# Performance work log

Hardware: AMD Instinct MI355X
Metric: run time of the kernel (lower is better)

The kernel has to match this reference:

```python
import jax, jax.numpy as jnp
import numpy as np

N = 1048576   # points
C = 50000     # clusters
F1, F2, FO = 128, 64, 64

def _lin(k, out_d, in_d):
    w = jax.random.normal(k, (out_d, in_d), jnp.float32) * (1.0 / np.sqrt(in_d))
    return w

def setup_inputs() -> dict:
    key = jax.random.key(0)
    ks = jax.random.split(key, 13)
    points = jax.random.normal(ks[0], (N, 3), jnp.float32)
    inv_feats = jax.random.normal(ks[1], (N, 4), jnp.float32)
    cluster = jax.random.randint(ks[2], (N,), 0, C, dtype=jnp.int32)
    return {
        "points": points, "inv_feats": inv_feats, "cluster": cluster,
        "W1": _lin(ks[3], F2, 4),       "b1": jnp.zeros((F2,), jnp.float32),
        "W2": _lin(ks[4], F1, F2),      "b2": jnp.zeros((F1,), jnp.float32),
        "W3": _lin(ks[5], F2, F1),      "b3": jnp.zeros((F2,), jnp.float32),
        "W4": _lin(ks[6], FO, F2),      "b4": jnp.zeros((FO,), jnp.float32),
        "W5": _lin(ks[7], 3, FO + 3),   "b5": jnp.zeros((3,), jnp.float32),
    }

def reference(points, inv_feats, cluster, W1, b1, W2, b2, W3, b3, W4, b4, W5, b5):
    relu = jax.nn.relu
    fc1 = relu(inv_feats @ W1.T + b1)                 # [N, F2]
    fc2 = relu(fc1 @ W2.T + b2)                       # [N, F1]
    # global_max_pool over clusters; fc2 >= 0 so clamping empty segments (-inf) to 0 is safe
    mx = jax.ops.segment_max(fc2, cluster, num_segments=C)
    mx = jnp.maximum(mx, 0.0)                         # [C, F1]
    fc3 = relu(mx @ W3.T + b3)                        # [C, F2]
    fc4 = relu(fc3 @ W4.T + b4)                       # [C, FO]
    repeated = fc4[cluster]                           # gather [N, FO]
    concat = jnp.concatenate([points, repeated], axis=-1)  # [N, FO+3]
    fc5 = relu(concat @ W5.T + b5)                    # [N, 3]
    sums = jax.ops.segment_sum(fc5, cluster, num_segments=C)
    cnt = jax.ops.segment_sum(jnp.ones((fc5.shape[0], 1), fc5.dtype), cluster, num_segments=C)
    angles = jax.nn.sigmoid(sums / jnp.maximum(cnt, 1.0))  # [C, 3]
    return (fc4, angles)
```

## Files before the change

kernel.cpp:

```cpp
#include <hip/hip_runtime.h>

#define N_PTS 1048576
#define NC 50000
#define SCAN_B 196

typedef int   i32x4  __attribute__((ext_vector_type(4)));
typedef float f32x4v __attribute__((ext_vector_type(4)));

__device__ __forceinline__ unsigned short bf16rne(float f) {
    unsigned u = __float_as_uint(f);
    u = (u + 0x7fffu + ((u >> 16) & 1u)) >> 16;
    return (unsigned short)u;
}
__device__ __forceinline__ f32x4v mfma16(i32x4 a, i32x4 b, f32x4v c) {
    asm("v_mfma_f32_16x16x32_bf16 %0, %1, %2, %0" : "+v"(c) : "v"(a), "v"(b));
    return c;
}
__device__ __forceinline__ int cvtpk(float lo, float hi) {
    int r;
    asm("v_cvt_pk_bf16_f32 %0, %1, %2" : "=v"(r) : "v"(lo), "v"(hi));
    return r;
}

#define DPPSHR(D, X) __builtin_amdgcn_update_dpp(0, (X), 0x110 | (D), 0xf, 0xf, true)
#define DPPSHL1(X)   __builtin_amdgcn_update_dpp(0, (X), 0x101, 0xf, 0xf, true)

__global__ __launch_bounds__(256) void k_histprep(
    const int* __restrict__ cluster, int* __restrict__ counts,
    const float* __restrict__ W2, const float* __restrict__ W3,
    const float* __restrict__ W4,
    unsigned short* __restrict__ W2bf, unsigned short* __restrict__ W3bf,
    unsigned short* __restrict__ W4bf)
{
    int i = blockIdx.x * 256 + threadIdx.x;
    if (i < 8192)       W2bf[i]         = bf16rne(W2[i]);
    else if (i < 16384) W3bf[i - 8192]  = bf16rne(W3[i - 8192]);
    else if (i < 20480) W4bf[i - 16384] = bf16rne(W4[i - 16384]);
    atomicAdd(counts + cluster[i], 1);
}

__device__ __forceinline__ int block_excl_scan256(int v, int* lsum, int tid) {
    const int lane = tid & 63, wv = tid >> 6;
    int x = v, u;
    u = __shfl_up(x, 1, 64);  if (lane >= 1)  x += u;
    u = __shfl_up(x, 2, 64);  if (lane >= 2)  x += u;
    u = __shfl_up(x, 4, 64);  if (lane >= 4)  x += u;
    u = __shfl_up(x, 8, 64);  if (lane >= 8)  x += u;
    u = __shfl_up(x, 16, 64); if (lane >= 16) x += u;
    u = __shfl_up(x, 32, 64); if (lane >= 32) x += u;
    if (lane == 63) lsum[wv] = x;
    __syncthreads();
    int woff = 0;
    if (wv > 0) woff += lsum[0];
    if (wv > 1) woff += lsum[1];
    if (wv > 2) woff += lsum[2];
    return woff + x - v;
}

__global__ __launch_bounds__(256) void k_scanA(
    const int* __restrict__ counts, int* __restrict__ partial)
{
    __shared__ int lsum[4];
    int i = blockIdx.x * 256 + threadIdx.x;
    int v = (i < NC) ? counts[i] : 0;
    int e = block_excl_scan256(v, lsum, threadIdx.x);
    if (threadIdx.x == 255) partial[blockIdx.x] = e + v;
}

__global__ __launch_bounds__(256) void k_scanC(
    const int* __restrict__ counts, const int* __restrict__ partial,
    int* __restrict__ cursor)
{
    __shared__ int lsum[4];
    __shared__ int tot;
    const int tid = threadIdx.x;
    int pv = (tid < SCAN_B && tid < blockIdx.x) ? partial[tid] : 0;
    int pe = block_excl_scan256(pv, lsum, tid);
    if (tid == 255) tot = pe + pv;
    __syncthreads();
    const int pref = tot;
    __syncthreads();
    int i = blockIdx.x * 256 + tid;
    int v = (i < NC) ? counts[i] : 0;
    int e = block_excl_scan256(v, lsum, tid);
    if (i < NC) cursor[i] = pref + e;
}

template<bool SORTED>
__global__ __launch_bounds__(256) void k_scatter(
    const int* __restrict__ cluster, const float* __restrict__ inv,
    const float* __restrict__ points, int* __restrict__ cursor,
    int* __restrict__ perm, int* __restrict__ pclus,
    float4* __restrict__ invs, float4* __restrict__ ptsc)
{
    int i = blockIdx.x * 256 + threadIdx.x;
    int c = cluster[i];
    int pos = atomicAdd(cursor + c, 1);
    pclus[pos] = c;
    if (SORTED) {
        invs[pos] = *(const float4*)(inv + (size_t)i * 4);
        float4 pt = { points[(size_t)i * 3 + 0], points[(size_t)i * 3 + 1],
                      points[(size_t)i * 3 + 2], 0.f };
        ptsc[pos] = pt;
    } else {
        perm[pos] = i;
    }
}

template<bool SORTED>
__global__ __launch_bounds__(256, 4) void k_points_mfma(
    const float* __restrict__ inv_feats,
    const int* __restrict__ perm, const int* __restrict__ pclus,
    const float4* __restrict__ invs,
    const float* __restrict__ W1, const float* __restrict__ b1,
    const unsigned short* __restrict__ W2bf, const float* __restrict__ b2,
    float* __restrict__ mx)
{
    const int tid  = threadIdx.x;
    const int wv   = tid >> 6;
    const int l    = tid & 63;
    const int base = (blockIdx.x * 4 + wv) * 32;
    const int m16 = l & 15;
    const int g4  = (l >> 4) * 4;
    const int k8  = (l >> 4) * 8;

    float4 xA, xB;
    if (SORTED) {
        xA = invs[base + m16];
        xB = invs[base + 16 + m16];
    } else {
        const int pA = perm[base + m16];
        const int pB = perm[base + 16 + m16];
        xA = *(const float4*)(inv_feats + (size_t)pA * 4);
        xB = *(const float4*)(inv_feats + (size_t)pB * 4);
    }

#define ROW2(K, QA, QB) float QA, QB; { \
    const float4 w = *(const float4*)(W1 + (size_t)(K) * 4); \
    const float bb = b1[K]; \
    float a = bb; \
    a = fmaf(w.x, xA.x, a); a = fmaf(w.y, xA.y, a); \
    a = fmaf(w.z, xA.z, a); a = fmaf(w.w, xA.w, a); \
    QA = fmaxf(a, 0.f); \
    float b = bb; \
    b = fmaf(w.x, xB.x, b); b = fmaf(w.y, xB.y, b); \
    b = fmaf(w.z, xB.z, b); b = fmaf(w.w, xB.w, b); \
    QB = fmaxf(b, 0.f); }

    i32x4 b00, b01, b10, b11;
    {
        ROW2(k8 + 0, qa0, qb0) ROW2(k8 + 1, qa1, qb1)
        ROW2(k8 + 2, qa2, qb2) ROW2(k8 + 3, qa3, qb3)
        ROW2(k8 + 4, qa4, qb4) ROW2(k8 + 5, qa5, qb5)
        ROW2(k8 + 6, qa6, qb6) ROW2(k8 + 7, qa7, qb7)
        b00[0] = cvtpk(qa0, qa1); b00[1] = cvtpk(qa2, qa3);
        b00[2] = cvtpk(qa4, qa5); b00[3] = cvtpk(qa6, qa7);
        b10[0] = cvtpk(qb0, qb1); b10[1] = cvtpk(qb2, qb3);
        b10[2] = cvtpk(qb4, qb5); b10[3] = cvtpk(qb6, qb7);
    }
    {
        ROW2(32 + k8 + 0, qa0, qb0) ROW2(32 + k8 + 1, qa1, qb1)
        ROW2(32 + k8 + 2, qa2, qb2) ROW2(32 + k8 + 3, qa3, qb3)
        ROW2(32 + k8 + 4, qa4, qb4) ROW2(32 + k8 + 5, qa5, qb5)
        ROW2(32 + k8 + 6, qa6, qb6) ROW2(32 + k8 + 7, qa7, qb7)
        b01[0] = cvtpk(qa0, qa1); b01[1] = cvtpk(qa2, qa3);
        b01[2] = cvtpk(qa4, qa5); b01[3] = cvtpk(qa6, qa7);
        b11[0] = cvtpk(qb0, qb1); b11[1] = cvtpk(qb2, qb3);
        b11[2] = cvtpk(qb4, qb5); b11[3] = cvtpk(qb6, qb7);
    }
#undef ROW2

    const int cp0 = pclus[base + m16] + 1;
    const int cp1 = pclus[base + 16 + m16] + 1;
    const bool e0a = (DPPSHR(1, cp0) == cp0);
    const bool e0b = (DPPSHR(2, cp0) == cp0);
    const bool e0c = (DPPSHR(4, cp0) == cp0);
    const bool e0d = (DPPSHR(8, cp0) == cp0);
    const bool tl0 = (DPPSHL1(cp0) != cp0);
    const bool e1a = (DPPSHR(1, cp1) == cp1);
    const bool e1b = (DPPSHR(2, cp1) == cp1);
    const bool e1c = (DPPSHR(4, cp1) == cp1);
    const bool e1d = (DPPSHR(8, cp1) == cp1);
    const bool tl1 = (DPPSHL1(cp1) != cp1);
    int* mrow0 = (int*)mx + (size_t)(cp0 - 1) * 128;
    int* mrow1 = (int*)mx + (size_t)(cp1 - 1) * 128;

#define LDA(MB, KK) (*(const i32x4*)(W2bf + (size_t)(kcc + (MB)*16 + m16) * 64 + (KK)*32 + k8))

#define SC4(V, EA, EB, EC, ED) { float _u; \
    _u = __int_as_float(DPPSHR(1, __float_as_int(V))); if (EA) V = fmaxf(V, _u); \
    _u = __int_as_float(DPPSHR(2, __float_as_int(V))); if (EB) V = fmaxf(V, _u); \
    _u = __int_as_float(DPPSHR(4, __float_as_int(V))); if (EC) V = fmaxf(V, _u); \
    _u = __int_as_float(DPPSHR(8, __float_as_int(V))); if (ED) V = fmaxf(V, _u); }

#define EMIT(ACC, MB, EA, EB, EC, ED, TL, MROW) { \
    const float4 bb = *(const float4*)(b2 + kcc + (MB)*16 + g4); \
    float v0 = fmaxf(ACC[0] + bb.x, 0.f); \
    float v1 = fmaxf(ACC[1] + bb.y, 0.f); \
    float v2 = fmaxf(ACC[2] + bb.z, 0.f); \
    float v3 = fmaxf(ACC[3] + bb.w, 0.f); \
    SC4(v0, EA, EB, EC, ED) SC4(v1, EA, EB, EC, ED) \
    SC4(v2, EA, EB, EC, ED) SC4(v3, EA, EB, EC, ED) \
    if (TL) { \
        if (v0 > 0.f) atomicMax(MROW + kcc + (MB)*16 + g4 + 0, __float_as_int(v0)); \
        if (v1 > 0.f) atomicMax(MROW + kcc + (MB)*16 + g4 + 1, __float_as_int(v1)); \
        if (v2 > 0.f) atomicMax(MROW + kcc + (MB)*16 + g4 + 2, __float_as_int(v2)); \
        if (v3 > 0.f) atomicMax(MROW + kcc + (MB)*16 + g4 + 3, __float_as_int(v3)); } }

#define PASS(KC) { \
    const int kcc = (KC) * 64; \
    const i32x4 a00 = LDA(0,0), a01 = LDA(0,1), a10 = LDA(1,0), a11 = LDA(1,1); \
    const i32x4 a20 = LDA(2,0), a21 = LDA(2,1), a30 = LDA(3,0), a31 = LDA(3,1); \
    f32x4v c00 = {0.f,0.f,0.f,0.f}, c01 = {0.f,0.f,0.f,0.f}; \
    f32x4v c10 = {0.f,0.f,0.f,0.f}, c11 = {0.f,0.f,0.f,0.f}; \
    f32x4v c20 = {0.f,0.f,0.f,0.f}, c21 = {0.f,0.f,0.f,0.f}; \
    f32x4v c30 = {0.f,0.f,0.f,0.f}, c31 = {0.f,0.f,0.f,0.f}; \
    c00 = mfma16(a00, b00, c00); c00 = mfma16(a01, b01, c00); \
    c10 = mfma16(a10, b00, c10); c10 = mfma16(a11, b01, c10); \
    c20 = mfma16(a20, b00, c20); c20 = mfma16(a21, b01, c20); \
    c30 = mfma16(a30, b00, c30); c30 = mfma16(a31, b01, c30); \
    c01 = mfma16(a00, b10, c01); c01 = mfma16(a01, b11, c01); \
    c11 = mfma16(a10, b10, c11); c11 = mfma16(a11, b11, c11); \
    c21 = mfma16(a20, b10, c21); c21 = mfma16(a21, b11, c21); \
    c31 = mfma16(a30, b10, c31); c31 = mfma16(a31, b11, c31); \
    EMIT(c00, 0, e0a, e0b, e0c, e0d, tl0, mrow0) \
    EMIT(c10, 1, e0a, e0b, e0c, e0d, tl0, mrow0) \
    EMIT(c20, 2, e0a, e0b, e0c, e0d, tl0, mrow0) \
    EMIT(c30, 3, e0a, e0b, e0c, e0d, tl0, mrow0) \
    EMIT(c01, 0, e1a, e1b, e1c, e1d, tl1, mrow1) \
    EMIT(c11, 1, e1a, e1b, e1c, e1d, tl1, mrow1) \
    EMIT(c21, 2, e1a, e1b, e1c, e1d, tl1, mrow1) \
    EMIT(c31, 3, e1a, e1b, e1c, e1d, tl1, mrow1) }

    PASS(0)
    PASS(1)
#undef PASS
#undef EMIT
#undef SC4
#undef LDA
}

__global__ __launch_bounds__(256, 4) void k_cluster_mfma(
    const float* __restrict__ mx,
    const unsigned short* __restrict__ W3bf, const float* __restrict__ b3,
    const unsigned short* __restrict__ W4bf, const float* __restrict__ b4,
    float* __restrict__ fc4out)
{
    __shared__ __align__(16) unsigned short f3[4][32 * 64];
    const int tid = threadIdx.x;
    const int wv  = tid >> 6;
    const int l   = tid & 63;
    const int m16 = l & 15;
    const int g4  = (l >> 4) * 4;
    const int k8  = (l >> 4) * 8;
    const int cbase = (blockIdx.x * 4 + wv) * 32;
    const int cA = cbase + m16;
    const int cB = cbase + 16 + m16;
    const size_t rA = (size_t)min(cA, NC - 1) * 128;
    const size_t rB = (size_t)min(cB, NC - 1) * 128;
    unsigned short* f3w = &f3[wv][0];
    const int swA = (m16 & 7) << 3;
    const int swB = swA;

    f32x4v d00 = {0,0,0,0}, d01 = {0,0,0,0}, d02 = {0,0,0,0}, d03 = {0,0,0,0};
    f32x4v d10 = {0,0,0,0}, d11 = {0,0,0,0}, d12 = {0,0,0,0}, d13 = {0,0,0,0};

#define LD3(MB, KK) (*(const i32x4*)(W3bf + (size_t)((MB)*16 + m16) * 128 + (KK)*32 + k8))
#define FC3STEP(KK) { \
    const float4 vA0 = *(const float4*)(mx + rA + (KK)*32 + k8); \
    const float4 vA1 = *(const float4*)(mx + rA + (KK)*32 + k8 + 4); \
    const float4 vB0 = *(const float4*)(mx + rB + (KK)*32 + k8); \
    const float4 vB1 = *(const float4*)(mx + rB + (KK)*32 + k8 + 4); \
    i32x4 bA = { cvtpk(vA0.x, vA0.y), cvtpk(vA0.z, vA0.w), \
                 cvtpk(vA1.x, vA1.y), cvtpk(vA1.z, vA1.w) }; \
    i32x4 bB = { cvtpk(vB0.x, vB0.y), cvtpk(vB0.z, vB0.w), \
                 cvtpk(vB1.x, vB1.y), cvtpk(vB1.z, vB1.w) }; \
    const i32x4 a0 = LD3(0, KK), a1 = LD3(1, KK), a2 = LD3(2, KK), a3 = LD3(3, KK); \
    d00 = mfma16(a0, bA, d00); d01 = mfma16(a1, bA, d01); \
    d02 = mfma16(a2, bA, d02); d03 = mfma16(a3, bA, d03); \
    d10 = mfma16(a0, bB, d10); d11 = mfma16(a1, bB, d11); \
    d12 = mfma16(a2, bB, d12); d13 = mfma16(a3, bB, d13); }
    FC3STEP(0) FC3STEP(1) FC3STEP(2) FC3STEP(3)
#undef FC3STEP
#undef LD3

#define ST3(DD, MB, CL, SW) { \
    const float4 bb = *(const float4*)(b3 + (MB)*16 + g4); \
    float v0 = fmaxf(DD[0] + bb.x, 0.f); \
    float v1 = fmaxf(DD[1] + bb.y, 0.f); \
    float v2 = fmaxf(DD[2] + bb.z, 0.f); \
    float v3 = fmaxf(DD[3] + bb.w, 0.f); \
    int2 pk = { cvtpk(v0, v1), cvtpk(v2, v3) }; \
    *(int2*)(f3w + (CL)*64 + ((((MB)*16 + g4)) ^ (SW))) = pk; }
    ST3(d00, 0, m16, swA) ST3(d01, 1, m16, swA) ST3(d02, 2, m16, swA) ST3(d03, 3, m16, swA)
    ST3(d10, 0, 16 + m16, swB) ST3(d11, 1, 16 + m16, swB) ST3(d12, 2, 16 + m16, swB) ST3(d13, 3, 16 + m16, swB)
#undef ST3

    f32x4v e00 = {0,0,0,0}, e01 = {0,0,0,0}, e02 = {0,0,0,0}, e03 = {0,0,0,0};
    f32x4v e10 = {0,0,0,0}, e11 = {0,0,0,0}, e12 = {0,0,0,0}, e13 = {0,0,0,0};
#define LD4(MB, KK) (*(const i32x4*)(W4bf + (size_t)((MB)*16 + m16) * 64 + (KK)*32 + k8))
#define FC4STEP(KK) { \
    const i32x4 bA4 = *(const i32x4*)(f3w + m16*64 + (((KK)*32 + k8) ^ swA)); \
    const i32x4 bB4 = *(const i32x4*)(f3w + (16 + m16)*64 + (((KK)*32 + k8) ^ swB)); \
    const i32x4 a0 = LD4(0, KK), a1 = LD4(1, KK), a2 = LD4(2, KK), a3 = LD4(3, KK); \
    e00 = mfma16(a0, bA4, e00); e01 = mfma16(a1, bA4, e01); \
    e02 = mfma16(a2, bA4, e02); e03 = mfma16(a3, bA4, e03); \
    e10 = mfma16(a0, bB4, e10); e11 = mfma16(a1, bB4, e11); \
    e12 = mfma16(a2, bB4, e12); e13 = mfma16(a3, bB4, e13); }
    FC4STEP(0) FC4STEP(1)
#undef FC4STEP
#undef LD4

#define WR(EE, MB, CL) if ((CL) < NC) { \
    const float4 bb = *(const float4*)(b4 + (MB)*16 + g4); \
    float4 o; \
    o.x = fmaxf(EE[0] + bb.x, 0.f); \
    o.y = fmaxf(EE[1] + bb.y, 0.f); \
    o.z = fmaxf(EE[2] + bb.z, 0.f); \
    o.w = fmaxf(EE[3] + bb.w, 0.f); \
    *(float4*)(fc4out + (size_t)(CL)*64 + (MB)*16 + g4) = o; }
    WR(e00, 0, cA) WR(e01, 1, cA) WR(e02, 2, cA) WR(e03, 3, cA)
    WR(e10, 0, cB) WR(e11, 1, cB) WR(e12, 2, cB) WR(e13, 3, cB)
#undef WR
}

template<bool SORTED>
__global__ __launch_bounds__(256) void k_fc5_sorted(
    const float* __restrict__ points,
    const int* __restrict__ perm, const int* __restrict__ pclus,
    const float4* __restrict__ ptsc,
    const float* __restrict__ fc4, const float* __restrict__ W5,
    const float* __restrict__ b5, float* __restrict__ sums)
{
    const int t = blockIdx.x * 256 + threadIdx.x;
    const int c = pclus[t];
    float p0, p1, p2;
    if (SORTED) {
        const float4 pt = ptsc[t];
        p0 = pt.x; p1 = pt.y; p2 = pt.z;
    } else {
        const int p = perm[t];
        p0 = points[(size_t)p * 3 + 0];
        p1 = points[(size_t)p * 3 + 1];
        p2 = points[(size_t)p * 3 + 2];
    }
    const float* f4 = fc4 + (size_t)c * 64;

    float a0 = b5[0];
    a0 = fmaf(W5[0], p0, a0); a0 = fmaf(W5[1], p1, a0); a0 = fmaf(W5[2], p2, a0);
    float a1 = b5[1];
    a1 = fmaf(W5[67], p0, a1); a1 = fmaf(W5[68], p1, a1); a1 = fmaf(W5[69], p2, a1);
    float a2 = b5[2];
    a2 = fmaf(W5[134], p0, a2); a2 = fmaf(W5[135], p1, a2); a2 = fmaf(W5[136], p2, a2);

#pragma unroll
    for (int j = 0; j < 64; j += 4) {
        float4 v = *(const float4*)(f4 + j);
        a0 = fmaf(W5[3 + j + 0], v.x, a0);
        a0 = fmaf(W5[3 + j + 1], v.y, a0);
        a0 = fmaf(W5[3 + j + 2], v.z, a0);
        a0 = fmaf(W5[3 + j + 3], v.w, a0);
        a1 = fmaf(W5[70 + j + 0], v.x, a1);
        a1 = fmaf(W5[70 + j + 1], v.y, a1);
        a1 = fmaf(W5[70 + j + 2], v.z, a1);
        a1 = fmaf(W5[70 + j + 3], v.w, a1);
        a2 = fmaf(W5[137 + j + 0], v.x, a2);
        a2 = fmaf(W5[137 + j + 1], v.y, a2);
        a2 = fmaf(W5[137 + j + 2], v.z, a2);
        a2 = fmaf(W5[137 + j + 3], v.w, a2);
    }
    a0 = fmaxf(a0, 0.f);
    a1 = fmaxf(a1, 0.f);
    a2 = fmaxf(a2, 0.f);

    const int lane = threadIdx.x & 63;
    const int cu1  = __shfl_up(c, 1, 64);
    const int cu2  = __shfl_up(c, 2, 64);
    const int cu4  = __shfl_up(c, 4, 64);
    const int cu8  = __shfl_up(c, 8, 64);
    const int cu16 = __shfl_up(c, 16, 64);
    const int cu32 = __shfl_up(c, 32, 64);
    const int cdn  = __shfl_down(c, 1, 64);
    const bool eq0 = (lane >= 1)  && (cu1  == c);
    const bool eq1 = (lane >= 2)  && (cu2  == c);
    const bool eq2 = (lane >= 4)  && (cu4  == c);
    const bool eq3 = (lane >= 8)  && (cu8  == c);
    const bool eq4 = (lane >= 16) && (cu16 == c);
    const bool eq5 = (lane >= 32) && (cu32 == c);
    const bool tail = (lane == 63) || (cdn != c);

    float u0, u1, u2;
    u0 = __shfl_up(a0, 1, 64);  u1 = __shfl_up(a1, 1, 64);  u2 = __shfl_up(a2, 1, 64);
    if (eq0) { a0 += u0; a1 += u1; a2 += u2; }
    u0 = __shfl_up(a0, 2, 64);  u1 = __shfl_up(a1, 2, 64);  u2 = __shfl_up(a2, 2, 64);
    if (eq1) { a0 += u0; a1 += u1; a2 += u2; }
    u0 = __shfl_up(a0, 4, 64);  u1 = __shfl_up(a1, 4, 64);  u2 = __shfl_up(a2, 4, 64);
    if (eq2) { a0 += u0; a1 += u1; a2 += u2; }
    u0 = __shfl_up(a0, 8, 64);  u1 = __shfl_up(a1, 8, 64);  u2 = __shfl_up(a2, 8, 64);
    if (eq3) { a0 += u0; a1 += u1; a2 += u2; }
    u0 = __shfl_up(a0, 16, 64); u1 = __shfl_up(a1, 16, 64); u2 = __shfl_up(a2, 16, 64);
    if (eq4) { a0 += u0; a1 += u1; a2 += u2; }
    u0 = __shfl_up(a0, 32, 64); u1 = __shfl_up(a1, 32, 64); u2 = __shfl_up(a2, 32, 64);
    if (eq5) { a0 += u0; a1 += u1; a2 += u2; }

    if (tail) {
        float* srow = sums + (size_t)c * 3;
        atomicAdd(srow + 0, a0);
        atomicAdd(srow + 1, a1);
        atomicAdd(srow + 2, a2);
    }
}

__global__ __launch_bounds__(256) void k_angles(
    const float* __restrict__ sums, const int* __restrict__ counts,
    float* __restrict__ angout)
{
    int c = blockIdx.x * 256 + threadIdx.x;
    if (c >= NC) return;
    const float cnt = fmaxf((float)counts[c], 1.f);
#pragma unroll
    for (int r = 0; r < 3; ++r) {
        float s = sums[(size_t)c * 3 + r] / cnt;
        angout[(size_t)c * 3 + r] = 1.f / (1.f + expf(-s));
    }
}

extern "C" void kernel_launch(void* const* d_in, const int* in_sizes, int n_in,
                              void* d_out, int out_size, void* d_ws, size_t ws_size,
                              hipStream_t stream) {
    const float* points  = (const float*)d_in[0];
    const float* inv     = (const float*)d_in[1];
    const int*   cluster = (const int*)d_in[2];
    const float* W1 = (const float*)d_in[3];
    const float* b1 = (const float*)d_in[4];
    const float* W2 = (const float*)d_in[5];
    const float* b2 = (const float*)d_in[6];
    const float* W3 = (const float*)d_in[7];
    const float* b3 = (const float*)d_in[8];
    const float* W4 = (const float*)d_in[9];
    const float* b4 = (const float*)d_in[10];
    const float* W5 = (const float*)d_in[11];
    const float* b5 = (const float*)d_in[12];

    float* out    = (float*)d_out;
    float* fc4out = out;
    float* angout = out + (size_t)NC * 64;

    int*   counts = (int*)d_ws;
    float* sums   = (float*)(counts + NC);
    float* mx     = sums + (size_t)NC * 3;
    int*   cursor = (int*)(mx + (size_t)NC * 128);
    int*   pclus  = cursor + NC;
    unsigned short* W2bf = (unsigned short*)(pclus + N_PTS);
    unsigned short* W3bf = W2bf + 8192;
    unsigned short* W4bf = W3bf + 8192;
    int*   partial = (int*)(W4bf + 4096);
    int*   perm    = partial + 256;
    float4* invs   = (float4*)(perm + N_PTS);
    float4* ptsc   = invs + N_PTS;
    const size_t needed_sorted = (size_t)((char*)(ptsc + N_PTS) - (char*)d_ws);
    const bool sorted_mode = ws_size >= needed_sorted;

    hipMemsetAsync(d_ws, 0, (size_t)(NC + NC * 3 + NC * 128) * sizeof(float), stream);

    k_histprep <<<N_PTS / 256, 256, 0, stream>>>(cluster, counts, W2, W3, W4, W2bf, W3bf, W4bf);
    k_scanA    <<<SCAN_B, 256, 0, stream>>>(counts, partial);
    k_scanC    <<<SCAN_B, 256, 0, stream>>>(counts, partial, cursor);
    if (sorted_mode) {
        k_scatter<true>     <<<N_PTS / 256, 256, 0, stream>>>(cluster, inv, points, cursor, perm, pclus, invs, ptsc);
        k_points_mfma<true> <<<N_PTS / 128, 256, 0, stream>>>(inv, perm, pclus, invs, W1, b1, W2bf, b2, mx);
    } else {
        k_scatter<false>    <<<N_PTS / 256, 256, 0, stream>>>(cluster, inv, points, cursor, perm, pclus, invs, ptsc);
        k_points_mfma<false><<<N_PTS / 128, 256, 0, stream>>>(inv, perm, pclus, invs, W1, b1, W2bf, b2, mx);
    }
    k_cluster_mfma <<<(NC + 127) / 128, 256, 0, stream>>>(mx, W3bf, b3, W4bf, b4, fc4out);
    if (sorted_mode) {
        k_fc5_sorted<true>  <<<N_PTS / 256, 256, 0, stream>>>(points, perm, pclus, ptsc, fc4out, W5, b5, sums);
    } else {
        k_fc5_sorted<false> <<<N_PTS / 256, 256, 0, stream>>>(points, perm, pclus, ptsc, fc4out, W5, b5, sums);
    }
    k_angles <<<(NC + 255) / 256, 256, 0, stream>>>(sums, counts, angout);
}
```

Measured before the change: 295.7 us.

## Assign one wavefront per cluster for fc1/fc2 and segment max in sorted mode

Adds a kernel that maps each wavefront to one cluster's contiguous run of sorted points. It iterates over 32-point tiles and runs fc1 plus the fc2 MFMA, keeping a running max in registers. A DPP reduction then writes the cluster max directly to mx, which avoids the per-point-tile boundary handling and atomic max traffic of the previous point-parallel kernel. The tradeoff is load imbalance across clusters of different sizes, wasted lanes on partial tiles (about 21 points per cluster on average, so often only one tile), and lower occupancy with launch bounds of 3.

```diff
diff --git a/kernel.cpp b/kernel.cpp
--- a/kernel.cpp
+++ b/kernel.cpp
@@ -3,9 +3,11 @@
 #define N_PTS 1048576
 #define NC 50000
 #define SCAN_B 196
+#define NBIG (-3.0e38f)
 
 typedef int   i32x4  __attribute__((ext_vector_type(4)));
 typedef float f32x4v __attribute__((ext_vector_type(4)));
+typedef short s16x8  __attribute__((ext_vector_type(8)));
 
 __device__ __forceinline__ unsigned short bf16rne(float f) {
     unsigned u = __float_as_uint(f);
@@ -15,6 +17,10 @@
 __device__ __forceinline__ f32x4v mfma16(i32x4 a, i32x4 b, f32x4v c) {
     asm("v_mfma_f32_16x16x32_bf16 %0, %1, %2, %0" : "+v"(c) : "v"(a), "v"(b));
     return c;
+}
+__device__ __forceinline__ f32x4v mfma16i(i32x4 a, i32x4 b, f32x4v c) {
+    return __builtin_amdgcn_mfma_f32_16x16x32_bf16(
+        __builtin_bit_cast(s16x8, a), __builtin_bit_cast(s16x8, b), c, 0, 0, 0);
 }
 __device__ __forceinline__ int cvtpk(float lo, float hi) {
     int r;
@@ -107,11 +113,140 @@
     }
 }
 
-template<bool SORTED>
+__global__ __launch_bounds__(256, 3) void k_points_cluster(
+    const float4* __restrict__ invs,
+    const int* __restrict__ counts, const int* __restrict__ cursor,
+    const float* __restrict__ W1, const float* __restrict__ b1,
+    const unsigned short* __restrict__ W2bf, const float* __restrict__ b2,
+    float* __restrict__ mx)
+{
+    const int tid = threadIdx.x;
+    const int wv  = tid >> 6;
+    const int l   = tid & 63;
+    const int c   = blockIdx.x * 4 + wv;
+    const int m16 = l & 15;
+    const int g4  = (l >> 4) * 4;
+    const int k8  = (l >> 4) * 8;
+
+    const int n     = counts[c];
+    const int start = cursor[c] - n;
+
+    f32x4v r00 = {NBIG,NBIG,NBIG,NBIG}, r01 = r00, r02 = r00, r03 = r00;
+    f32x4v r10 = r00, r11 = r00, r12 = r00, r13 = r00;
+
+#define ROW2(K, QA, QB) float QA, QB; { \
+    const float4 w = *(const float4*)(W1 + (size_t)(K) * 4); \
+    const float bb = b1[K]; \
+    float a = bb; \
+    a = fmaf(w.x, xA.x, a); a = fmaf(w.y, xA.y, a); \
+    a = fmaf(w.z, xA.z, a); a = fmaf(w.w, xA.w, a); \
+    QA = fmaxf(a, 0.f); \
+    float b = bb; \
+    b = fmaf(w.x, xB.x, b); b = fmaf(w.y, xB.y, b); \
+    b = fmaf(w.z, xB.z, b); b = fmaf(w.w, xB.w, b); \
+    QB = fmaxf(b, 0.f); }
+
+#define LDA(MB, KK) (*(const i32x4*)(W2bf + (size_t)(kcc + (MB)*16 + m16) * 64 + (KK)*32 + k8))
+
+#define MERGE(RUN, CA, CB) { \
+    float _a, _b; \
+    _a = VA ? CA[0] : NBIG; _b = VB ? CB[0] : NBIG; RUN[0] = fmaxf(RUN[0], fmaxf(_a, _b)); \
+    _a = VA ? CA[1] : NBIG; _b = VB ? CB[1] : NBIG; RUN[1] = fmaxf(RUN[1], fmaxf(_a, _b)); \
+    _a = VA ? CA[2] : NBIG; _b = VB ? CB[2] : NBIG; RUN[2] = fmaxf(RUN[2], fmaxf(_a, _b)); \
+    _a = VA ? CA[3] : NBIG; _b = VB ? CB[3] : NBIG; RUN[3] = fmaxf(RUN[3], fmaxf(_a, _b)); }
+
+#define PASSC(KC, R0, R1, R2, R3) { \
+    const int kcc = (KC) * 64; \
+    const i32x4 a00 = LDA(0,0), a01 = LDA(0,1), a10 = LDA(1,0), a11 = LDA(1,1); \
+    const i32x4 a20 = LDA(2,0), a21 = LDA(2,1), a30 = LDA(3,0), a31 = LDA(3,1); \
+    f32x4v c00 = {0.f,0.f,0.f,0.f}, c01 = {0.f,0.f,0.f,0.f}; \
+    f32x4v c10 = {0.f,0.f,0.f,0.f}, c11 = {0.f,0.f,0.f,0.f}; \
+    f32x4v c20 = {0.f,0.f,0.f,0.f}, c21 = {0.f,0.f,0.f,0.f}; \
+    f32x4v c30 = {0.f,0.f,0.f,0.f}, c31 = {0.f,0.f,0.f,0.f}; \
+    c00 = mfma16i(a00, b00, c00); c00 = mfma16i(a01, b01, c00); \
+    c10 = mfma16i(a10, b00, c10); c10 = mfma16i(a11, b01, c10); \
+    c20 = mfma16i(a20, b00, c20); c20 = mfma16i(a21, b01, c20); \
+    c30 = mfma16i(a30, b00, c30); c30 = mfma16i(a31, b01, c30); \
+    c01 = mfma16i(a00, b10, c01); c01 = mfma16i(a01, b11, c01); \
+    c11 = mfma16i(a10, b10, c11); c11 = mfma16i(a11, b11, c11); \
+    c21 = mfma16i(a20, b10, c21); c21 = mfma16i(a21, b11, c21); \
+    c31 = mfma16i(a30, b10, c31); c31 = mfma16i(a31, b11, c31); \
+    MERGE(R0, c00, c01) MERGE(R1, c10, c11) \
+    MERGE(R2, c20, c21) MERGE(R3, c30, c31) }
+
+    const int tmax = (n + 31) >> 5;
+    for (int t = 0; t < tmax; ++t) {
+        const int p0 = t * 32 + m16;
+        const int p1 = t * 32 + 16 + m16;
+        const bool VA = p0 < n;
+        const bool VB = p1 < n;
+        const float4 xA = invs[min(start + p0, N_PTS - 1)];
+        const float4 xB = invs[min(start + p1, N_PTS - 1)];
+
+        i32x4 b00, b01, b10, b11;
+        {
+            ROW2(k8 + 0, qa0, qb0) ROW2(k8 + 1, qa1, qb1)
+            ROW2(k8 + 2, qa2, qb2) ROW2(k8 + 3, qa3, qb3)
+            ROW2(k8 + 4, qa4, qb4) ROW2(k8 + 5, qa5, qb5)
+            ROW2(k8 + 6, qa6, qb6) ROW2(k8 + 7, qa7, qb7)
+            b00[0] = cvtpk(qa0, qa1); b00[1] = cvtpk(qa2, qa3);
+            b00[2] = cvtpk(qa4, qa5); b00[3] = cvtpk(qa6, qa7);
+            b10[0] = cvtpk(qb0, qb1); b10[1] = cvtpk(qb2, qb3);
+            b10[2] = cvtpk(qb4, qb5); b10[3] = cvtpk(qb6, qb7);
+        }
+        {
+            ROW2(32 + k8 + 0, qa0, qb0) ROW2(32 + k8 + 1, qa1, qb1)
+            ROW2(32 + k8 + 2, qa2, qb2) ROW2(32 + k8 + 3, qa3, qb3)
+            ROW2(32 + k8 + 4, qa4, qb4) ROW2(32 + k8 + 5, qa5, qb5)
+            ROW2(32 + k8 + 6, qa6, qb6) ROW2(32 + k8 + 7, qa7, qb7)
+            b01[0] = cvtpk(qa0, qa1); b01[1] = cvtpk(qa2, qa3);
+            b01[2] = cvtpk(qa4, qa5); b01[3] = cvtpk(qa6, qa7);
+            b11[0] = cvtpk(qb0, qb1); b11[1] = cvtpk(qb2, qb3);
+            b11[2] = cvtpk(qb4, qb5); b11[3] = cvtpk(qb6, qb7);
+        }
+        PASSC(0, r00, r01, r02, r03)
+        PASSC(1, r10, r11, r12, r13)
+    }
+
+#define EMITF(RUN, MB, KCC) { \
+    const float4 bb = *(const float4*)(b2 + (KCC) + (MB)*16 + g4); \
+    float v0 = fmaxf(RUN[0] + bb.x, 0.f); \
+    float v1 = fmaxf(RUN[1] + bb.y, 0.f); \
+    float v2 = fmaxf(RUN[2] + bb.z, 0.f); \
+    float v3 = fmaxf(RUN[3] + bb.w, 0.f); \
+    float _u; \
+    _u = __int_as_float(DPPSHR(1, __float_as_int(v0))); v0 = fmaxf(v0, _u); \
+    _u = __int_as_float(DPPSHR(1, __float_as_int(v1))); v1 = fmaxf(v1, _u); \
+    _u = __int_as_float(DPPSHR(1, __float_as_int(v2))); v2 = fmaxf(v2, _u); \
+    _u = __int_as_float(DPPSHR(1, __float_as_int(v3))); v3 = fmaxf(v3, _u); \
+    _u = __int_as_float(DPPSHR(2, __float_as_int(v0))); v0 = fmaxf(v0, _u); \
+    _u = __int_as_float(DPPSHR(2, __float_as_int(v1))); v1 = fmaxf(v1, _u); \
+    _u = __int_as_float(DPPSHR(2, __float_as_int(v2))); v2 = fmaxf(v2, _u); \
+    _u = __int_as_float(DPPSHR(2, __float_as_int(v3))); v3 = fmaxf(v3, _u); \
+    _u = __int_as_float(DPPSHR(4, __float_as_int(v0))); v0 = fmaxf(v0, _u); \
+    _u = __int_as_float(DPPSHR(4, __float_as_int(v1))); v1 = fmaxf(v1, _u); \
+    _u = __int_as_float(DPPSHR(4, __float_as_int(v2))); v2 = fmaxf(v2, _u); \
+    _u = __int_as_float(DPPSHR(4, __float_as_int(v3))); v3 = fmaxf(v3, _u); \
+    _u = __int_as_float(DPPSHR(8, __float_as_int(v0))); v0 = fmaxf(v0, _u); \
+    _u = __int_as_float(DPPSHR(8, __float_as_int(v1))); v1 = fmaxf(v1, _u); \
+    _u = __int_as_float(DPPSHR(8, __float_as_int(v2))); v2 = fmaxf(v2, _u); \
+    _u = __int_as_float(DPPSHR(8, __float_as_int(v3))); v3 = fmaxf(v3, _u); \
+    if (m16 == 15) { \
+        float4 o = { v0, v1, v2, v3 }; \
+        *(float4*)(mx + (size_t)c * 128 + (KCC) + (MB)*16 + g4) = o; } }
+
+    EMITF(r00, 0, 0)  EMITF(r01, 1, 0)  EMITF(r02, 2, 0)  EMITF(r03, 3, 0)
+    EMITF(r10, 0, 64) EMITF(r11, 1, 64) EMITF(r12, 2, 64) EMITF(r13, 3, 64)
+#undef EMITF
+#undef PASSC
+#undef MERGE
+#undef LDA
+#undef ROW2
+}
+
 __global__ __launch_bounds__(256, 4) void k_points_mfma(
     const float* __restrict__ inv_feats,
     const int* __restrict__ perm, const int* __restrict__ pclus,
-    const float4* __restrict__ invs,
     const float* __restrict__ W1, const float* __restrict__ b1,
     const unsigned short* __restrict__ W2bf, const float* __restrict__ b2,
     float* __restrict__ mx)
@@ -124,16 +259,10 @@
     const int g4  = (l >> 4) * 4;
     const int k8  = (l >> 4) * 8;
 
-    float4 xA, xB;
-    if (SORTED) {
-        xA = invs[base + m16];
-        xB = invs[base + 16 + m16];
-    } else {
-        const int pA = perm[base + m16];
-        const int pB = perm[base + 16 + m16];
-        xA = *(const float4*)(inv_feats + (size_t)pA * 4);
-        xB = *(const float4*)(inv_feats + (size_t)pB * 4);
-    }
+    const int pA = perm[base + m16];
+    const int pB = perm[base + 16 + m16];
+    const float4 xA = *(const float4*)(inv_feats + (size_t)pA * 4);
+    const float4 xB = *(const float4*)(inv_feats + (size_t)pB * 4);
 
 #define ROW2(K, QA, QB) float QA, QB; { \
     const float4 w = *(const float4*)(W1 + (size_t)(K) * 4); \
@@ -467,11 +596,11 @@
     k_scanA    <<<SCAN_B, 256, 0, stream>>>(counts, partial);
     k_scanC    <<<SCAN_B, 256, 0, stream>>>(counts, partial, cursor);
     if (sorted_mode) {
-        k_scatter<true>     <<<N_PTS / 256, 256, 0, stream>>>(cluster, inv, points, cursor, perm, pclus, invs, ptsc);
-        k_points_mfma<true> <<<N_PTS / 128, 256, 0, stream>>>(inv, perm, pclus, invs, W1, b1, W2bf, b2, mx);
+        k_scatter<true>    <<<N_PTS / 256, 256, 0, stream>>>(cluster, inv, points, cursor, perm, pclus, invs, ptsc);
+        k_points_cluster   <<<NC / 4, 256, 0, stream>>>(invs, counts, cursor, W1, b1, W2bf, b2, mx);
     } else {
-        k_scatter<false>    <<<N_PTS / 256, 256, 0, stream>>>(cluster, inv, points, cursor, perm, pclus, invs, ptsc);
-        k_points_mfma<false><<<N_PTS / 128, 256, 0, stream>>>(inv, perm, pclus, invs, W1, b1, W2bf, b2, mx);
+        k_scatter<false>   <<<N_PTS / 256, 256, 0, stream>>>(cluster, inv, points, cursor, perm, pclus, invs, ptsc);
+        k_points_mfma      <<<N_PTS / 128, 256, 0, stream>>>(inv, perm, pclus, W1, b1, W2bf, b2, mx);
     }
     k_cluster_mfma <<<(NC + 127) / 128, 256, 0, stream>>>(mx, W3bf, b3, W4bf, b4, fc4out);
     if (sorted_mode) {
```

New measurement: 331.8 us. 12.2% more time.
